# Performance work log

Measured on AMD Instinct MI355X. Metric: run time of the kernel, lower is better.

The kernel has to match this reference:

```python
import jax, jax.numpy as jnp
import numpy as np
from jax.ops import segment_sum

N = 100_000     # num nodes
E = 1_600_000   # num edges
G = 1024        # num graphs in batch
DIN, H, EMB, L = 128, 128, 64, 3
EPS = 1e-5


def setup_inputs() -> dict:
    key = jax.random.key(0)
    ks = jax.random.split(key, 12)
    x = jax.random.normal(ks[0], (N, DIN), dtype=jnp.float32)
    edge_index = jax.random.randint(ks[1], (2, E), 0, N, dtype=jnp.int32)
    batch = jnp.sort(jax.random.randint(ks[2], (N,), 0, G, dtype=jnp.int32))
    s = 0.05
    W_in = jax.random.normal(ks[3], (DIN, H), dtype=jnp.float32) * s
    b_in = jnp.zeros((H,), dtype=jnp.float32)
    Ws = jax.random.normal(ks[4], (L, H, H), dtype=jnp.float32) * s
    bs = jnp.zeros((L, H), dtype=jnp.float32)
    gammas = jnp.ones((L, H), dtype=jnp.float32)
    betas = jnp.zeros((L, H), dtype=jnp.float32)
    W1 = jax.random.normal(ks[5], (H, H), dtype=jnp.float32) * s
    b1 = jnp.zeros((H,), dtype=jnp.float32)
    W2 = jax.random.normal(ks[6], (H, EMB), dtype=jnp.float32) * s
    b2 = jnp.zeros((EMB,), dtype=jnp.float32)
    return {"x": x, "edge_index": edge_index, "batch": batch,
            "W_in": W_in, "b_in": b_in, "Ws": Ws, "bs": bs,
            "gammas": gammas, "betas": betas,
            "W1": W1, "b1": b1, "W2": W2, "b2": b2}


def reference(x, edge_index, batch, W_in, b_in, Ws, bs, gammas, betas, W1, b1, W2, b2):
    src, dst = edge_index[0], edge_index[1]
    # GCN normalization with implicit self-loops: deg = in-degree + 1
    deg = segment_sum(jnp.ones((E,), x.dtype), dst, num_segments=N) + 1.0
    dinv = jax.lax.rsqrt(deg)                      # deg^{-1/2}, [N]
    edge_norm = (dinv[src] * dinv[dst])[:, None]   # [E,1]
    self_norm = (dinv * dinv)[:, None]             # [N,1] = 1/deg

    h = jax.nn.relu(x @ W_in + b_in)               # input projection (dropout=0 / eval)
    for i in range(L):
        hw = h @ Ws[i]                             # [N,H] linear transform
        agg = segment_sum(hw[src] * edge_norm, dst, num_segments=N)
        h = agg + hw * self_norm + bs[i]           # GCNConv output (self-loop term fused)
        # BatchNorm1d over node dim (training-mode batch statistics)
        mean = jnp.mean(h, axis=0)
        var = jnp.var(h, axis=0)
        h = (h - mean) * jax.lax.rsqrt(var + EPS) * gammas[i] + betas[i]
        h = jax.nn.relu(h)

    # global mean pool per graph
    cnt = segment_sum(jnp.ones((N,), x.dtype), batch, num_segments=G)
    pooled = segment_sum(h, batch, num_segments=G) / jnp.maximum(cnt, 1.0)[:, None]

    out = jax.nn.relu(pooled @ W1 + b1) @ W2 + b2  # [G, EMB]
    return out
```

## Files before the change

### kernel.cpp

```cpp
#include <hip/hip_runtime.h>

#define HD 128
#define EMB 64
#define EPS 1e-5f

typedef __bf16 bf16x8 __attribute__((ext_vector_type(8)));
typedef float f32x4 __attribute__((ext_vector_type(4)));

__device__ __forceinline__ float4 ld4(const float* p) {
    return *reinterpret_cast<const float4*>(p);
}

__device__ __forceinline__ unsigned short f2bf(float f) {
    unsigned u = __float_as_uint(f);
    u += 0x7FFF + ((u >> 16) & 1);
    return (unsigned short)(u >> 16);
}
__device__ __forceinline__ float bf2f(unsigned short b) {
    return __uint_as_float((unsigned)b << 16);
}
__device__ __forceinline__ float blo(unsigned u) { return __uint_as_float(u << 16); }
__device__ __forceinline__ float bhi(unsigned u) { return __uint_as_float(u & 0xffff0000u); }
__device__ __forceinline__ unsigned pk2(float a, float b) {
    return (unsigned)f2bf(a) | ((unsigned)f2bf(b) << 16);
}

__global__ void k_hist(const int* __restrict__ dst, int* __restrict__ deg, int e) {
    int i = blockIdx.x * blockDim.x + threadIdx.x;
    if (i < e) atomicAdd(&deg[dst[i]], 1);
}

__global__ void k_dinv(const int* __restrict__ deg, float* __restrict__ dinv, int n) {
    int i = blockIdx.x * blockDim.x + threadIdx.x;
    if (i < n) dinv[i] = 1.0f / sqrtf((float)deg[i] + 1.0f);
}

__global__ void k_scan_part(const int* __restrict__ deg, int* __restrict__ out,
                            int* __restrict__ bsum, int n) {
    __shared__ int s[256];
    int i = blockIdx.x * 256 + threadIdx.x;
    int v = (i < n) ? deg[i] : 0;
    s[threadIdx.x] = v;
    __syncthreads();
    #pragma unroll
    for (int off = 1; off < 256; off <<= 1) {
        int t = (threadIdx.x >= off) ? s[threadIdx.x - off] : 0;
        __syncthreads();
        s[threadIdx.x] += t;
        __syncthreads();
    }
    if (i < n) out[i] = s[threadIdx.x] - v;
    if (threadIdx.x == 255) bsum[blockIdx.x] = s[255];
}

__global__ void k_scan_mid(int* __restrict__ bsum, int nb) {
    __shared__ int s[512];
    int t = threadIdx.x;
    int v = (t < nb) ? bsum[t] : 0;
    s[t] = v;
    __syncthreads();
    for (int off = 1; off < 512; off <<= 1) {
        int u = (t >= off) ? s[t - off] : 0;
        __syncthreads();
        s[t] += u;
        __syncthreads();
    }
    if (t < nb) bsum[t] = s[t] - v;
}

__global__ void k_scan_add(int* __restrict__ rs, const int* __restrict__ bsum,
                           int n, int e_total) {
    int i = blockIdx.x * 256 + threadIdx.x;
    if (i < n) rs[i] += bsum[blockIdx.x];
    if (i == 0) rs[n] = e_total;
}

__global__ void k_scatter(const int* __restrict__ src, const int* __restrict__ dst,
                          int* __restrict__ cursor, int* __restrict__ csr_src, int e) {
    int i = blockIdx.x * blockDim.x + threadIdx.x;
    if (i < e) {
        int d = dst[i];
        int pos = atomicAdd(&cursor[d], 1);
        csr_src[pos] = src[i];
    }
}

__global__ void k_wprep(const float* __restrict__ W_in, const float* __restrict__ Ws,
                        unsigned short* __restrict__ wt) {
    int m = blockIdx.x >> 7;
    int nn = blockIdx.x & 127;
    int k = threadIdx.x;
    const float* src = (m == 0) ? W_in : Ws + (size_t)(m - 1) * 16384;
    wt[(size_t)m * 16384 + nn * 128 + k] = f2bf(src[k * 128 + nn]);
}

template <bool APPLY_BN, bool OUT_BIAS_RELU, bool OUT_BF16>
__global__ __launch_bounds__(256) void k_gemm(
        const float* __restrict__ A, const unsigned short* __restrict__ Wt,
        const float* __restrict__ bias,
        const float* __restrict__ aff_a, const float* __restrict__ aff_b,
        void* __restrict__ Cout, int M) {
    __shared__ char sA[64 * 256];
    __shared__ char sB[128 * 256];
    const int tid = threadIdx.x;
    const int row0 = blockIdx.x * 64;

    #pragma unroll
    for (int it = 0; it < 8; ++it) {
        int idx = it * 256 + tid;
        int r = idx >> 4, c = idx & 15;
        uint4 v = reinterpret_cast<const uint4*>(Wt)[idx];
        int byte = r * 256 + c * 16;
        *reinterpret_cast<uint4*>(sB + (byte ^ ((r & 7) << 4))) = v;
    }
    #pragma unroll
    for (int it = 0; it < 4; ++it) {
        int idx = it * 256 + tid;
        int r = idx >> 4, c = idx & 15;
        int gm = row0 + r;
        float4 v0 = make_float4(0.f, 0.f, 0.f, 0.f), v1 = v0;
        if (gm < M) {
            v0 = ld4(A + (size_t)gm * HD + c * 8);
            v1 = ld4(A + (size_t)gm * HD + c * 8 + 4);
        }
        if (APPLY_BN) {
            float4 a0 = ld4(aff_a + c * 8), a1 = ld4(aff_a + c * 8 + 4);
            float4 b0 = ld4(aff_b + c * 8), b1 = ld4(aff_b + c * 8 + 4);
            v0.x = fmaxf(fmaf(v0.x, a0.x, b0.x), 0.f);
            v0.y = fmaxf(fmaf(v0.y, a0.y, b0.y), 0.f);
            v0.z = fmaxf(fmaf(v0.z, a0.z, b0.z), 0.f);
            v0.w = fmaxf(fmaf(v0.w, a0.w, b0.w), 0.f);
            v1.x = fmaxf(fmaf(v1.x, a1.x, b1.x), 0.f);
            v1.y = fmaxf(fmaf(v1.y, a1.y, b1.y), 0.f);
            v1.z = fmaxf(fmaf(v1.z, a1.z, b1.z), 0.f);
            v1.w = fmaxf(fmaf(v1.w, a1.w, b1.w), 0.f);
        }
        uint4 pk;
        pk.x = pk2(v0.x, v0.y); pk.y = pk2(v0.z, v0.w);
        pk.z = pk2(v1.x, v1.y); pk.w = pk2(v1.z, v1.w);
        int byte = r * 256 + c * 16;
        *reinterpret_cast<uint4*>(sA + (byte ^ ((r & 7) << 4))) = pk;
    }
    __syncthreads();

    const int wave = tid >> 6;
    const int lane = tid & 63;
    const int l15 = lane & 15;
    const int kq  = lane >> 4;

    bf16x8 af[4];
    {
        int arow = wave * 16 + l15;
        int base = arow * 256;
        int sw = (arow & 7) << 4;
        #pragma unroll
        for (int ks = 0; ks < 4; ++ks) {
            int byte = base + kq * 16 + ks * 64;
            af[ks] = __builtin_bit_cast(bf16x8,
                *reinterpret_cast<const uint4*>(sA + (byte ^ sw)));
        }
    }

    #pragma unroll
    for (int nt = 0; nt < 8; ++nt) {
        int bcol = nt * 16 + l15;
        int bbase = bcol * 256;
        int bsw = (bcol & 7) << 4;
        f32x4 c = {0.f, 0.f, 0.f, 0.f};
        #pragma unroll
        for (int ks = 0; ks < 4; ++ks) {
            int byte = bbase + kq * 16 + ks * 64;
            bf16x8 bf = __builtin_bit_cast(bf16x8,
                *reinterpret_cast<const uint4*>(sB + (byte ^ bsw)));
            c = __builtin_amdgcn_mfma_f32_16x16x32_bf16(af[ks], bf, c, 0, 0, 0);
        }
        int col = nt * 16 + l15;
        int grbase = row0 + wave * 16 + kq * 4;
        if (OUT_BF16) {
            unsigned short* C16 = (unsigned short*)Cout;
            #pragma unroll
            for (int i = 0; i < 4; ++i) {
                int gr = grbase + i;
                if (gr < M) C16[(size_t)gr * HD + col] = f2bf(c[i]);
            }
        } else {
            float* C32 = (float*)Cout;
            float bb = OUT_BIAS_RELU ? bias[col] : 0.f;
            #pragma unroll
            for (int i = 0; i < 4; ++i) {
                int gr = grbase + i;
                float o = c[i];
                if (OUT_BIAS_RELU) o = fmaxf(o + bb, 0.f);
                if (gr < M) C32[(size_t)gr * HD + col] = o;
            }
        }
    }
}

#define NPB 8
__global__ void k_agg(const unsigned short* __restrict__ hw, const int* __restrict__ row_start,
                      const int* __restrict__ csr_src, const float* __restrict__ dinv,
                      const float* __restrict__ bias_row, float* __restrict__ h_pre,
                      float* __restrict__ colsum, float* __restrict__ colsumsq, int n) {
    const int tid  = threadIdx.x;
    const int lane = tid & 63;
    const int slot = tid >> 6;
    const int q    = lane & 15;
    const int grp  = lane >> 4;
    const int n0 = blockIdx.x * (4 * NPB);
    const uint4* __restrict__ hw4 = (const uint4*)hw;

    float b8[8];
    #pragma unroll
    for (int k = 0; k < 8; ++k) b8[k] = bias_row[q * 8 + k];

    float psum8[8], psq8[8];
    #pragma unroll
    for (int k = 0; k < 8; ++k) { psum8[k] = 0.f; psq8[k] = 0.f; }

    for (int nn = 0; nn < NPB; ++nn) {
        int node = n0 + nn * 4 + slot;
        if (node >= n) continue;
        float dn = dinv[node];
        float acc[8];
        #pragma unroll
        for (int k = 0; k < 8; ++k) acc[k] = 0.f;

        const int jb = row_start[node], je = row_start[node + 1];
        for (int j = jb; j < je; j += 8) {
            int e0 = j + grp;
            int s0 = (e0 < je) ? csr_src[e0] : 0;
            float w0 = (e0 < je) ? dinv[s0] * dn : 0.f;
            uint4 r0 = hw4[(size_t)s0 * 16 + q];
            int e1 = j + 4 + grp;
            int s1 = (e1 < je) ? csr_src[e1] : 0;
            float w1 = (e1 < je) ? dinv[s1] * dn : 0.f;
            uint4 r1 = hw4[(size_t)s1 * 16 + q];

            acc[0] = fmaf(blo(r0.x), w0, acc[0]); acc[1] = fmaf(bhi(r0.x), w0, acc[1]);
            acc[2] = fmaf(blo(r0.y), w0, acc[2]); acc[3] = fmaf(bhi(r0.y), w0, acc[3]);
            acc[4] = fmaf(blo(r0.z), w0, acc[4]); acc[5] = fmaf(bhi(r0.z), w0, acc[5]);
            acc[6] = fmaf(blo(r0.w), w0, acc[6]); acc[7] = fmaf(bhi(r0.w), w0, acc[7]);

            acc[0] = fmaf(blo(r1.x), w1, acc[0]); acc[1] = fmaf(bhi(r1.x), w1, acc[1]);
            acc[2] = fmaf(blo(r1.y), w1, acc[2]); acc[3] = fmaf(bhi(r1.y), w1, acc[3]);
            acc[4] = fmaf(blo(r1.z), w1, acc[4]); acc[5] = fmaf(bhi(r1.z), w1, acc[5]);
            acc[6] = fmaf(blo(r1.w), w1, acc[6]); acc[7] = fmaf(bhi(r1.w), w1, acc[7]);
        }

        #pragma unroll
        for (int k = 0; k < 8; ++k) acc[k] += __shfl_xor(acc[k], 16, 64);
        #pragma unroll
        for (int k = 0; k < 8; ++k) acc[k] += __shfl_xor(acc[k], 32, 64);

        uint4 ow = hw4[(size_t)node * 16 + q];
        float sn = dn * dn;
        acc[0] = fmaf(blo(ow.x), sn, acc[0] + b8[0]);
        acc[1] = fmaf(bhi(ow.x), sn, acc[1] + b8[1]);
        acc[2] = fmaf(blo(ow.y), sn, acc[2] + b8[2]);
        acc[3] = fmaf(bhi(ow.y), sn, acc[3] + b8[3]);
        acc[4] = fmaf(blo(ow.z), sn, acc[4] + b8[4]);
        acc[5] = fmaf(bhi(ow.z), sn, acc[5] + b8[5]);
        acc[6] = fmaf(blo(ow.w), sn, acc[6] + b8[6]);
        acc[7] = fmaf(bhi(ow.w), sn, acc[7] + b8[7]);

        if (grp == 0) {
            float* dst = h_pre + (size_t)node * HD + q * 8;
            *reinterpret_cast<float4*>(dst)     = make_float4(acc[0], acc[1], acc[2], acc[3]);
            *reinterpret_cast<float4*>(dst + 4) = make_float4(acc[4], acc[5], acc[6], acc[7]);
            #pragma unroll
            for (int k = 0; k < 8; ++k) {
                psum8[k] += acc[k];
                psq8[k] = fmaf(acc[k], acc[k], psq8[k]);
            }
        }
    }

    __shared__ float redS[4][128];
    __shared__ float redQ[4][128];
    if (grp == 0) {
        #pragma unroll
        for (int k = 0; k < 8; ++k) {
            redS[slot][q * 8 + k] = psum8[k];
            redQ[slot][q * 8 + k] = psq8[k];
        }
    }
    __syncthreads();
    int f = tid & 127;
    if (tid < 128) {
        float s = redS[0][f] + redS[1][f] + redS[2][f] + redS[3][f];
        atomicAdd(&colsum[f], s);
    } else {
        float s = redQ[0][f] + redQ[1][f] + redQ[2][f] + redQ[3][f];
        atomicAdd(&colsumsq[f], s);
    }
}

__global__ void k_bncoef(float* __restrict__ colsum, float* __restrict__ colsumsq,
                         const float* __restrict__ gamma, const float* __restrict__ beta,
                         float* __restrict__ aff_a, float* __restrict__ aff_b, int n) {
    int f = threadIdx.x;
    float inv_n = 1.0f / (float)n;
    float mean = colsum[f] * inv_n;
    float var = colsumsq[f] * inv_n - mean * mean;
    float rstd = 1.0f / sqrtf(var + EPS);
    float a = gamma[f] * rstd;
    aff_a[f] = a;
    aff_b[f] = beta[f] - mean * a;
    colsum[f] = 0.f;
    colsumsq[f] = 0.f;
}

__global__ void k_gbounds(const int* __restrict__ batch, int* __restrict__ gstart,
                          int n, int g) {
    int gi = blockIdx.x * blockDim.x + threadIdx.x;
    if (gi > g) return;
    int lo = 0, hi = n;
    while (lo < hi) {
        int mid = (lo + hi) >> 1;
        if (batch[mid] < gi) lo = mid + 1; else hi = mid;
    }
    gstart[gi] = lo;
}

__global__ void k_pool(const float* __restrict__ h_pre, const int* __restrict__ gstart,
                       const float* __restrict__ aff_a, const float* __restrict__ aff_b,
                       float* __restrict__ pooled) {
    const int gi = blockIdx.x;
    const int tid = threadIdx.x;
    const int lane = tid & 63;
    const int half = tid >> 6;
    const float2* __restrict__ h2 = (const float2*)h_pre;
    const float2 a2 = *((const float2*)aff_a + lane);
    const float2 b2 = *((const float2*)aff_b + lane);
    int s = gstart[gi], e = gstart[gi + 1];
    float2 sum = make_float2(0.f, 0.f);
    for (int i = s + half; i < e; i += 2) {
        float2 v = h2[(size_t)i * 64 + lane];
        sum.x += fmaxf(fmaf(v.x, a2.x, b2.x), 0.f);
        sum.y += fmaxf(fmaf(v.y, a2.y, b2.y), 0.f);
    }
    __shared__ float2 red[128];
    red[tid] = sum;
    __syncthreads();
    if (half == 0) {
        float2 o = red[tid + 64];
        sum.x += o.x; sum.y += o.y;
        float inv = 1.0f / fmaxf((float)(e - s), 1.0f);
        float2* p2 = (float2*)pooled;
        p2[(size_t)gi * 64 + lane] = make_float2(sum.x * inv, sum.y * inv);
    }
}

__global__ void k_head(const float* __restrict__ pooled, const float* __restrict__ W1,
                       const float* __restrict__ b1, const float* __restrict__ W2,
                       const float* __restrict__ b2, float* __restrict__ out) {
    __shared__ float p[HD];
    __shared__ float t[HD];
    int gi = blockIdx.x;
    int j = threadIdx.x;
    p[j] = pooled[(size_t)gi * HD + j];
    __syncthreads();
    float acc = b1[j];
    #pragma unroll 8
    for (int k = 0; k < HD; ++k) acc = fmaf(p[k], W1[(size_t)k * HD + j], acc);
    t[j] = fmaxf(acc, 0.f);
    __syncthreads();
    if (j < EMB) {
        float o = b2[j];
        #pragma unroll 8
        for (int k = 0; k < HD; ++k) o = fmaf(t[k], W2[(size_t)k * EMB + j], o);
        out[(size_t)gi * EMB + j] = o;
    }
}

extern "C" void kernel_launch(void* const* d_in, const int* in_sizes, int n_in,
                              void* d_out, int out_size, void* d_ws, size_t ws_size,
                              hipStream_t stream) {
    const float* x     = (const float*)d_in[0];
    const int*   ei    = (const int*)d_in[1];
    const int*   batch = (const int*)d_in[2];
    const float* W_in  = (const float*)d_in[3];
    const float* b_in  = (const float*)d_in[4];
    const float* Ws    = (const float*)d_in[5];
    const float* bs    = (const float*)d_in[6];
    const float* gam   = (const float*)d_in[7];
    const float* bet   = (const float*)d_in[8];
    const float* W1    = (const float*)d_in[9];
    const float* b1    = (const float*)d_in[10];
    const float* W2    = (const float*)d_in[11];
    const float* b2    = (const float*)d_in[12];
    float* out = (float*)d_out;

    const int n = in_sizes[0] / HD;
    const int e = in_sizes[1] / 2;
    const int g = out_size / EMB;

    const int* esrc = ei;
    const int* edst = ei + e;

    char* w = (char*)d_ws;
    auto alloc = [&](size_t bytes) {
        char* p = w;
        w += (bytes + 255) & ~(size_t)255;
        return p;
    };
    float* hbuf             = (float*)alloc((size_t)n * HD * 4);
    unsigned short* hw      = (unsigned short*)alloc((size_t)n * HD * 2);
    unsigned short* wtbuf   = (unsigned short*)alloc((size_t)4 * HD * HD * 2);
    int*   csr_src = (int*)alloc((size_t)e * 4);
    int*   deg     = (int*)alloc((size_t)n * 4);
    float* dinv    = (float*)alloc((size_t)n * 4);
    int*   rstart  = (int*)alloc((size_t)(n + 1) * 4);
    int*   cursor  = (int*)alloc((size_t)n * 4);
    int*   bsum    = (int*)alloc(512 * 4);
    float* colsum  = (float*)alloc(256 * 4);
    float* colsumsq = colsum + HD;
    float* aff_a   = (float*)alloc(256 * 4);
    float* aff_b   = aff_a + HD;
    int*   gstart  = (int*)alloc((size_t)(g + 1) * 4);
    float* pooled  = (float*)alloc((size_t)g * HD * 4);

    hipMemsetAsync(deg, 0, (size_t)n * 4, stream);
    hipMemsetAsync(colsum, 0, 256 * 4, stream);

    const int eb = (e + 255) / 256;
    const int nb = (n + 255) / 256;

    k_wprep<<<512, 128, 0, stream>>>(W_in, Ws, wtbuf);
    k_hist<<<eb, 256, 0, stream>>>(edst, deg, e);
    k_dinv<<<nb, 256, 0, stream>>>(deg, dinv, n);
    k_scan_part<<<nb, 256, 0, stream>>>(deg, rstart, bsum, n);
    k_scan_mid<<<1, 512, 0, stream>>>(bsum, nb);
    k_scan_add<<<nb, 256, 0, stream>>>(rstart, bsum, n, e);
    hipMemcpyAsync(cursor, rstart, (size_t)n * 4, hipMemcpyDeviceToDevice, stream);
    k_scatter<<<eb, 256, 0, stream>>>(esrc, edst, cursor, csr_src, e);

    const int gb = (n + 63) / 64;
    k_gemm<false, true, false><<<gb, 256, 0, stream>>>(
        x, wtbuf, b_in, nullptr, nullptr, hbuf, n);

    const int ab = (n + 4 * NPB - 1) / (4 * NPB);
    for (int i = 0; i < 3; ++i) {
        if (i == 0)
            k_gemm<false, false, true><<<gb, 256, 0, stream>>>(
                hbuf, wtbuf + (size_t)(i + 1) * HD * HD, nullptr, nullptr, nullptr, hw, n);
        else
            k_gemm<true, false, true><<<gb, 256, 0, stream>>>(
                hbuf, wtbuf + (size_t)(i + 1) * HD * HD, nullptr, aff_a, aff_b, hw, n);
        k_agg<<<ab, 256, 0, stream>>>(hw, rstart, csr_src, dinv, bs + (size_t)i * HD,
                                      hbuf, colsum, colsumsq, n);
        k_bncoef<<<1, HD, 0, stream>>>(colsum, colsumsq, gam + (size_t)i * HD,
                                       bet + (size_t)i * HD, aff_a, aff_b, n);
    }

    k_gbounds<<<(g + 256) / 256, 256, 0, stream>>>(batch, gstart, n, g);
    k_pool<<<g, 128, 0, stream>>>(hbuf, gstart, aff_a, aff_b, pooled);
    k_head<<<g, HD, 0, stream>>>(pooled, W1, b1, W2, b2, out);
}
```

Before: 837.7 us.

## Fuse BN coefficients into consumers, merge pool/head, enlarge GEMM tile

Removes the k_bncoef launches by computing batch-norm scale and shift inside each consumer kernel, using per-layer column-sum buffers so no reset is needed. Merges the pooling and MLP head into one tail kernel and writes the CSR cursor inside the scan kernel instead of doing a separate device copy. The GEMM now processes 128 rows per block and reads B fragments directly from global memory instead of staging them in LDS. The aim is fewer launches and less LDS traffic, at the cost of redundant per-block coefficient math and uncached-in-LDS weight reads.

```diff
diff --git a/kernel.cpp b/kernel.cpp
--- a/kernel.cpp
+++ b/kernel.cpp
@@ -15,9 +15,6 @@
     unsigned u = __float_as_uint(f);
     u += 0x7FFF + ((u >> 16) & 1);
     return (unsigned short)(u >> 16);
-}
-__device__ __forceinline__ float bf2f(unsigned short b) {
-    return __uint_as_float((unsigned)b << 16);
 }
 __device__ __forceinline__ float blo(unsigned u) { return __uint_as_float(u << 16); }
 __device__ __forceinline__ float bhi(unsigned u) { return __uint_as_float(u & 0xffff0000u); }
@@ -68,10 +65,14 @@
     if (t < nb) bsum[t] = s[t] - v;
 }
 
-__global__ void k_scan_add(int* __restrict__ rs, const int* __restrict__ bsum,
-                           int n, int e_total) {
+__global__ void k_scan_add(int* __restrict__ rs, int* __restrict__ cursor,
+                           const int* __restrict__ bsum, int n, int e_total) {
     int i = blockIdx.x * 256 + threadIdx.x;
-    if (i < n) rs[i] += bsum[blockIdx.x];
+    if (i < n) {
+        int v = rs[i] + bsum[blockIdx.x];
+        rs[i] = v;
+        cursor[i] = v;
+    }
     if (i == 0) rs[n] = e_total;
 }
 
@@ -98,23 +99,28 @@
 __global__ __launch_bounds__(256) void k_gemm(
         const float* __restrict__ A, const unsigned short* __restrict__ Wt,
         const float* __restrict__ bias,
-        const float* __restrict__ aff_a, const float* __restrict__ aff_b,
-        void* __restrict__ Cout, int M) {
-    __shared__ char sA[64 * 256];
-    __shared__ char sB[128 * 256];
+        const float* __restrict__ gamma, const float* __restrict__ beta,
+        const float* __restrict__ colsum, const float* __restrict__ colsumsq,
+        float inv_n, void* __restrict__ Cout, int M) {
+    __shared__ char sA[128 * 256];
+    __shared__ float s_affa[HD], s_affb[HD];
     const int tid = threadIdx.x;
-    const int row0 = blockIdx.x * 64;
+    const int row0 = blockIdx.x * 128;
+
+    if (APPLY_BN) {
+        if (tid < HD) {
+            float mean = colsum[tid] * inv_n;
+            float var = colsumsq[tid] * inv_n - mean * mean;
+            float rstd = 1.0f / sqrtf(var + EPS);
+            float a = gamma[tid] * rstd;
+            s_affa[tid] = a;
+            s_affb[tid] = beta[tid] - mean * a;
+        }
+        __syncthreads();
+    }
 
     #pragma unroll
     for (int it = 0; it < 8; ++it) {
-        int idx = it * 256 + tid;
-        int r = idx >> 4, c = idx & 15;
-        uint4 v = reinterpret_cast<const uint4*>(Wt)[idx];
-        int byte = r * 256 + c * 16;
-        *reinterpret_cast<uint4*>(sB + (byte ^ ((r & 7) << 4))) = v;
-    }
-    #pragma unroll
-    for (int it = 0; it < 4; ++it) {
         int idx = it * 256 + tid;
         int r = idx >> 4, c = idx & 15;
         int gm = row0 + r;
@@ -124,16 +130,15 @@
             v1 = ld4(A + (size_t)gm * HD + c * 8 + 4);
         }
         if (APPLY_BN) {
-            float4 a0 = ld4(aff_a + c * 8), a1 = ld4(aff_a + c * 8 + 4);
-            float4 b0 = ld4(aff_b + c * 8), b1 = ld4(aff_b + c * 8 + 4);
-            v0.x = fmaxf(fmaf(v0.x, a0.x, b0.x), 0.f);
-            v0.y = fmaxf(fmaf(v0.y, a0.y, b0.y), 0.f);
-            v0.z = fmaxf(fmaf(v0.z, a0.z, b0.z), 0.f);
-            v0.w = fmaxf(fmaf(v0.w, a0.w, b0.w), 0.f);
-            v1.x = fmaxf(fmaf(v1.x, a1.x, b1.x), 0.f);
-            v1.y = fmaxf(fmaf(v1.y, a1.y, b1.y), 0.f);
-            v1.z = fmaxf(fmaf(v1.z, a1.z, b1.z), 0.f);
-            v1.w = fmaxf(fmaf(v1.w, a1.w, b1.w), 0.f);
+            int f0 = c * 8;
+            v0.x = fmaxf(fmaf(v0.x, s_affa[f0 + 0], s_affb[f0 + 0]), 0.f);
+            v0.y = fmaxf(fmaf(v0.y, s_affa[f0 + 1], s_affb[f0 + 1]), 0.f);
+            v0.z = fmaxf(fmaf(v0.z, s_affa[f0 + 2], s_affb[f0 + 2]), 0.f);
+            v0.w = fmaxf(fmaf(v0.w, s_affa[f0 + 3], s_affb[f0 + 3]), 0.f);
+            v1.x = fmaxf(fmaf(v1.x, s_affa[f0 + 4], s_affb[f0 + 4]), 0.f);
+            v1.y = fmaxf(fmaf(v1.y, s_affa[f0 + 5], s_affb[f0 + 5]), 0.f);
+            v1.z = fmaxf(fmaf(v1.z, s_affa[f0 + 6], s_affb[f0 + 6]), 0.f);
+            v1.w = fmaxf(fmaf(v1.w, s_affa[f0 + 7], s_affb[f0 + 7]), 0.f);
         }
         uint4 pk;
         pk.x = pk2(v0.x, v0.y); pk.y = pk2(v0.z, v0.w);
@@ -148,50 +153,54 @@
     const int l15 = lane & 15;
     const int kq  = lane >> 4;
 
-    bf16x8 af[4];
-    {
-        int arow = wave * 16 + l15;
+    bf16x8 af[2][4];
+    #pragma unroll
+    for (int mt = 0; mt < 2; ++mt) {
+        int arow = wave * 32 + mt * 16 + l15;
         int base = arow * 256;
         int sw = (arow & 7) << 4;
         #pragma unroll
         for (int ks = 0; ks < 4; ++ks) {
             int byte = base + kq * 16 + ks * 64;
-            af[ks] = __builtin_bit_cast(bf16x8,
+            af[mt][ks] = __builtin_bit_cast(bf16x8,
                 *reinterpret_cast<const uint4*>(sA + (byte ^ sw)));
         }
     }
 
+    const uint4* __restrict__ Wt4 = (const uint4*)Wt;
     #pragma unroll
     for (int nt = 0; nt < 8; ++nt) {
-        int bcol = nt * 16 + l15;
-        int bbase = bcol * 256;
-        int bsw = (bcol & 7) << 4;
-        f32x4 c = {0.f, 0.f, 0.f, 0.f};
+        int wrow = nt * 16 + l15;
+        f32x4 c0 = {0.f, 0.f, 0.f, 0.f};
+        f32x4 c1 = {0.f, 0.f, 0.f, 0.f};
         #pragma unroll
         for (int ks = 0; ks < 4; ++ks) {
-            int byte = bbase + kq * 16 + ks * 64;
-            bf16x8 bf = __builtin_bit_cast(bf16x8,
-                *reinterpret_cast<const uint4*>(sB + (byte ^ bsw)));
-            c = __builtin_amdgcn_mfma_f32_16x16x32_bf16(af[ks], bf, c, 0, 0, 0);
+            bf16x8 bf = __builtin_bit_cast(bf16x8, Wt4[wrow * 16 + ks * 4 + kq]);
+            c0 = __builtin_amdgcn_mfma_f32_16x16x32_bf16(af[0][ks], bf, c0, 0, 0, 0);
+            c1 = __builtin_amdgcn_mfma_f32_16x16x32_bf16(af[1][ks], bf, c1, 0, 0, 0);
         }
         int col = nt * 16 + l15;
-        int grbase = row0 + wave * 16 + kq * 4;
-        if (OUT_BF16) {
-            unsigned short* C16 = (unsigned short*)Cout;
-            #pragma unroll
-            for (int i = 0; i < 4; ++i) {
-                int gr = grbase + i;
-                if (gr < M) C16[(size_t)gr * HD + col] = f2bf(c[i]);
-            }
-        } else {
-            float* C32 = (float*)Cout;
-            float bb = OUT_BIAS_RELU ? bias[col] : 0.f;
-            #pragma unroll
-            for (int i = 0; i < 4; ++i) {
-                int gr = grbase + i;
-                float o = c[i];
-                if (OUT_BIAS_RELU) o = fmaxf(o + bb, 0.f);
-                if (gr < M) C32[(size_t)gr * HD + col] = o;
+        #pragma unroll
+        for (int mt = 0; mt < 2; ++mt) {
+            f32x4 c = mt ? c1 : c0;
+            int grbase = row0 + wave * 32 + mt * 16 + kq * 4;
+            if (OUT_BF16) {
+                unsigned short* C16 = (unsigned short*)Cout;
+                #pragma unroll
+                for (int i = 0; i < 4; ++i) {
+                    int gr = grbase + i;
+                    if (gr < M) C16[(size_t)gr * HD + col] = f2bf(c[i]);
+                }
+            } else {
+                float* C32 = (float*)Cout;
+                float bb = OUT_BIAS_RELU ? bias[col] : 0.f;
+                #pragma unroll
+                for (int i = 0; i < 4; ++i) {
+                    int gr = grbase + i;
+                    float o = c[i];
+                    if (OUT_BIAS_RELU) o = fmaxf(o + bb, 0.f);
+                    if (gr < M) C32[(size_t)gr * HD + col] = o;
+                }
             }
         }
     }
@@ -296,21 +305,6 @@
     }
 }
 
-__global__ void k_bncoef(float* __restrict__ colsum, float* __restrict__ colsumsq,
-                         const float* __restrict__ gamma, const float* __restrict__ beta,
-                         float* __restrict__ aff_a, float* __restrict__ aff_b, int n) {
-    int f = threadIdx.x;
-    float inv_n = 1.0f / (float)n;
-    float mean = colsum[f] * inv_n;
-    float var = colsumsq[f] * inv_n - mean * mean;
-    float rstd = 1.0f / sqrtf(var + EPS);
-    float a = gamma[f] * rstd;
-    aff_a[f] = a;
-    aff_b[f] = beta[f] - mean * a;
-    colsum[f] = 0.f;
-    colsumsq[f] = 0.f;
-}
-
 __global__ void k_gbounds(const int* __restrict__ batch, int* __restrict__ gstart,
                           int n, int g) {
     int gi = blockIdx.x * blockDim.x + threadIdx.x;
@@ -323,54 +317,62 @@
     gstart[gi] = lo;
 }
 
-__global__ void k_pool(const float* __restrict__ h_pre, const int* __restrict__ gstart,
-                       const float* __restrict__ aff_a, const float* __restrict__ aff_b,
-                       float* __restrict__ pooled) {
+__global__ __launch_bounds__(128) void k_tail(
+        const float* __restrict__ h_pre, const int* __restrict__ gstart,
+        const float* __restrict__ colsum, const float* __restrict__ colsumsq,
+        float inv_n, const float* __restrict__ gamma, const float* __restrict__ beta,
+        const float* __restrict__ W1, const float* __restrict__ b1,
+        const float* __restrict__ W2, const float* __restrict__ b2,
+        float* __restrict__ out) {
+    __shared__ float s_a[HD], s_b[HD];
+    __shared__ float2 red[128];
+    __shared__ float p[HD], t[HD];
     const int gi = blockIdx.x;
     const int tid = threadIdx.x;
+
+    {
+        float mean = colsum[tid] * inv_n;
+        float var = colsumsq[tid] * inv_n - mean * mean;
+        float rstd = 1.0f / sqrtf(var + EPS);
+        float a = gamma[tid] * rstd;
+        s_a[tid] = a;
+        s_b[tid] = beta[tid] - mean * a;
+    }
+    __syncthreads();
+
     const int lane = tid & 63;
     const int half = tid >> 6;
     const float2* __restrict__ h2 = (const float2*)h_pre;
-    const float2 a2 = *((const float2*)aff_a + lane);
-    const float2 b2 = *((const float2*)aff_b + lane);
+    const float2 a2 = make_float2(s_a[lane * 2], s_a[lane * 2 + 1]);
+    const float2 b2v = make_float2(s_b[lane * 2], s_b[lane * 2 + 1]);
     int s = gstart[gi], e = gstart[gi + 1];
     float2 sum = make_float2(0.f, 0.f);
     for (int i = s + half; i < e; i += 2) {
         float2 v = h2[(size_t)i * 64 + lane];
-        sum.x += fmaxf(fmaf(v.x, a2.x, b2.x), 0.f);
-        sum.y += fmaxf(fmaf(v.y, a2.y, b2.y), 0.f);
-    }
-    __shared__ float2 red[128];
+        sum.x += fmaxf(fmaf(v.x, a2.x, b2v.x), 0.f);
+        sum.y += fmaxf(fmaf(v.y, a2.y, b2v.y), 0.f);
+    }
     red[tid] = sum;
     __syncthreads();
     if (half == 0) {
         float2 o = red[tid + 64];
         sum.x += o.x; sum.y += o.y;
         float inv = 1.0f / fmaxf((float)(e - s), 1.0f);
-        float2* p2 = (float2*)pooled;
-        p2[(size_t)gi * 64 + lane] = make_float2(sum.x * inv, sum.y * inv);
-    }
-}
-
-__global__ void k_head(const float* __restrict__ pooled, const float* __restrict__ W1,
-                       const float* __restrict__ b1, const float* __restrict__ W2,
-                       const float* __restrict__ b2, float* __restrict__ out) {
-    __shared__ float p[HD];
-    __shared__ float t[HD];
-    int gi = blockIdx.x;
-    int j = threadIdx.x;
-    p[j] = pooled[(size_t)gi * HD + j];
-    __syncthreads();
-    float acc = b1[j];
+        p[lane * 2]     = sum.x * inv;
+        p[lane * 2 + 1] = sum.y * inv;
+    }
+    __syncthreads();
+
+    float acc = b1[tid];
     #pragma unroll 8
-    for (int k = 0; k < HD; ++k) acc = fmaf(p[k], W1[(size_t)k * HD + j], acc);
-    t[j] = fmaxf(acc, 0.f);
-    __syncthreads();
-    if (j < EMB) {
-        float o = b2[j];
+    for (int k = 0; k < HD; ++k) acc = fmaf(p[k], W1[(size_t)k * HD + tid], acc);
+    t[tid] = fmaxf(acc, 0.f);
+    __syncthreads();
+    if (tid < EMB) {
+        float o = b2[tid];
         #pragma unroll 8
-        for (int k = 0; k < HD; ++k) o = fmaf(t[k], W2[(size_t)k * EMB + j], o);
-        out[(size_t)gi * EMB + j] = o;
+        for (int k = 0; k < HD; ++k) o = fmaf(t[k], W2[(size_t)k * EMB + tid], o);
+        out[(size_t)gi * EMB + tid] = o;
     }
 }
 
@@ -395,6 +397,7 @@
     const int n = in_sizes[0] / HD;
     const int e = in_sizes[1] / 2;
     const int g = out_size / EMB;
+    const float inv_n = 1.0f / (float)n;
 
     const int* esrc = ei;
     const int* edst = ei + e;
@@ -414,15 +417,11 @@
     int*   rstart  = (int*)alloc((size_t)(n + 1) * 4);
     int*   cursor  = (int*)alloc((size_t)n * 4);
     int*   bsum    = (int*)alloc(512 * 4);
-    float* colsum  = (float*)alloc(256 * 4);
-    float* colsumsq = colsum + HD;
-    float* aff_a   = (float*)alloc(256 * 4);
-    float* aff_b   = aff_a + HD;
+    float* csbuf   = (float*)alloc(3 * 256 * 4);
     int*   gstart  = (int*)alloc((size_t)(g + 1) * 4);
-    float* pooled  = (float*)alloc((size_t)g * HD * 4);
 
     hipMemsetAsync(deg, 0, (size_t)n * 4, stream);
-    hipMemsetAsync(colsum, 0, 256 * 4, stream);
+    hipMemsetAsync(csbuf, 0, 3 * 256 * 4, stream);
 
     const int eb = (e + 255) / 256;
     const int nb = (n + 255) / 256;
@@ -432,29 +431,33 @@
     k_dinv<<<nb, 256, 0, stream>>>(deg, dinv, n);
     k_scan_part<<<nb, 256, 0, stream>>>(deg, rstart, bsum, n);
     k_scan_mid<<<1, 512, 0, stream>>>(bsum, nb);
-    k_scan_add<<<nb, 256, 0, stream>>>(rstart, bsum, n, e);
-    hipMemcpyAsync(cursor, rstart, (size_t)n * 4, hipMemcpyDeviceToDevice, stream);
+    k_scan_add<<<nb, 256, 0, stream>>>(rstart, cursor, bsum, n, e);
     k_scatter<<<eb, 256, 0, stream>>>(esrc, edst, cursor, csr_src, e);
 
-    const int gb = (n + 63) / 64;
+    const int gb = (n + 127) / 128;
     k_gemm<false, true, false><<<gb, 256, 0, stream>>>(
-        x, wtbuf, b_in, nullptr, nullptr, hbuf, n);
+        x, wtbuf, b_in, nullptr, nullptr, nullptr, nullptr, 0.f, hbuf, n);
 
     const int ab = (n + 4 * NPB - 1) / (4 * NPB);
     for (int i = 0; i < 3; ++i) {
+        float* cs = csbuf + (size_t)i * 256;
         if (i == 0)
             k_gemm<false, false, true><<<gb, 256, 0, stream>>>(
-                hbuf, wtbuf + (size_t)(i + 1) * HD * HD, nullptr, nullptr, nullptr, hw, n);
-        else
+                hbuf, wtbuf + (size_t)(i + 1) * HD * HD, nullptr,
+                nullptr, nullptr, nullptr, nullptr, 0.f, hw, n);
+        else {
+            float* csp = csbuf + (size_t)(i - 1) * 256;
             k_gemm<true, false, true><<<gb, 256, 0, stream>>>(
-                hbuf, wtbuf + (size_t)(i + 1) * HD * HD, nullptr, aff_a, aff_b, hw, n);
+                hbuf, wtbuf + (size_t)(i + 1) * HD * HD, nullptr,
+                gam + (size_t)(i - 1) * HD, bet + (size_t)(i - 1) * HD,
+                csp, csp + HD, inv_n, hw, n);
+        }
         k_agg<<<ab, 256, 0, stream>>>(hw, rstart, csr_src, dinv, bs + (size_t)i * HD,
-                                      hbuf, colsum, colsumsq, n);
-        k_bncoef<<<1, HD, 0, stream>>>(colsum, colsumsq, gam + (size_t)i * HD,
-                                       bet + (size_t)i * HD, aff_a, aff_b, n);
+                                      hbuf, cs, cs + HD, n);
     }
 
     k_gbounds<<<(g + 256) / 256, 256, 0, stream>>>(batch, gstart, n, g);
-    k_pool<<<g, 128, 0, stream>>>(hbuf, gstart, aff_a, aff_b, pooled);
-    k_head<<<g, HD, 0, stream>>>(pooled, W1, b1, W2, b2, out);
-}
+    float* cs2 = csbuf + 2 * 256;
+    k_tail<<<g, 128, 0, stream>>>(hbuf, gstart, cs2, cs2 + HD, inv_n,
+                                  gam + 2 * HD, bet + 2 * HD, W1, b1, W2, b2, out);
+}
```

Result: slower. 856.8 us (+2.3%).
